# Optimization experiments

Measured on AMD Instinct MI355X. Metric: run time of the kernel, lower is better.

Reference implementation:

```python
import jax, jax.numpy as jnp
import numpy as np

N = 65536   # nodes
D = 64      # feature dim
K = 32      # top-k kept features per node (k_value)
DEG = 16    # average degree
E = N * DEG # edges


def setup_inputs() -> dict:
    key = jax.random.key(0)
    k1, k2, k3, k4, k5 = jax.random.split(key, 5)
    feat = jax.random.normal(k1, (N, D), dtype=jnp.float32)
    topk_values = jax.random.normal(k2, (N, K), dtype=jnp.float32)
    topk_indices = jax.random.randint(k3, (N, K), 0, D, dtype=jnp.int32)
    edge_src = jax.random.randint(k4, (E,), 0, N, dtype=jnp.int32)
    # sorted dst row ids == CSR row structure (expanded indptr)
    edge_dst = jnp.sort(jax.random.randint(k5, (E,), 0, N, dtype=jnp.int32))
    eps = jnp.zeros((1,), dtype=jnp.float32)  # init_eps=0, learn_eps=False
    return {"feat": feat, "topk_values": topk_values, "eps": eps,
            "topk_indices": topk_indices, "edge_src": edge_src, "edge_dst": edge_dst}


def reference(feat, topk_values, eps, topk_indices, edge_src, edge_dst):
    n, d = feat.shape
    # MaxK SpMM: reconstruct sparse (top-k compressed) dense features, then
    # CSR sum-aggregation with unit edge values (graph_values = ones).
    rows = jnp.arange(n, dtype=topk_indices.dtype)[:, None]        # [N,1]
    dense = jnp.zeros_like(feat).at[rows, topk_indices].add(topk_values)  # [N,D]
    # neigh[i] = sum_{j in N(i)} dense[j]
    neigh = jax.ops.segment_sum(dense[edge_src], edge_dst, num_segments=n)  # [N,D]
    # GIN update: (1 + eps) * feat_dst + neigh  (apply_func=None, activation=None)
    return (1.0 + eps) * feat + neigh
```

## Files before the change

kernel.cpp:

```cpp
#include <hip/hip_runtime.h>


#define DFEAT 64
#define KTOP  32

__device__ __forceinline__ unsigned short f2bf(float x) {
    unsigned u = __float_as_uint(x);
    u += 0x7fffu + ((u >> 16) & 1u);
    return (unsigned short)(u >> 16);
}
__device__ __forceinline__ float bfu(unsigned int u16) {
    return __uint_as_float(u16 << 16);
}

__global__ __launch_bounds__(256) void prep_kernel(
    const float* __restrict__ topk_v,
    const int*   __restrict__ topk_i,
    const int*   __restrict__ edge_dst,
    unsigned int* __restrict__ dense16,
    int*          __restrict__ indptr,
    int n_nodes, int n_edges)
{
    __shared__ float rows[4][2 * DFEAT];
    int tid    = blockIdx.x * blockDim.x + threadIdx.x;
    int stride = gridDim.x * blockDim.x;
    int lane   = threadIdx.x & 63;
    int wid    = threadIdx.x >> 6;
    int wave   = tid >> 6;
    int nwaves = stride >> 6;
    int half   = lane >> 5;

    for (int e = tid; e < n_edges; e += stride) {
        int cur  = edge_dst[e];
        int prev = (e == 0) ? -1 : edge_dst[e - 1];
        for (int node = prev + 1; node <= cur; ++node) indptr[node] = e;
        if (e == n_edges - 1) {
            for (int node = cur + 1; node <= n_nodes; ++node) indptr[node] = n_edges;
        }
    }

    int total_pairs = n_nodes >> 1;
    for (int pair = wave; pair < total_pairs; pair += nwaves) {
        int nodeA = pair * 2;

        rows[wid][lane]      = 0.0f;
        rows[wid][lane + 64] = 0.0f;

        size_t base = (size_t)nodeA * KTOP;
        int   idx = topk_i[base + lane];
        float val = topk_v[base + lane];
        atomicAdd(&rows[wid][half * DFEAT + idx], val);

        float a = rows[wid][2 * lane];
        float b = rows[wid][2 * lane + 1];
        dense16[nodeA * 32 + lane] =
            (unsigned int)f2bf(a) | ((unsigned int)f2bf(b) << 16);
    }
}

__global__ __launch_bounds__(256) void aggregate_bf16_kernel(
    const uint4*  __restrict__ d16q,
    const float4* __restrict__ feat4,
    const float*  __restrict__ eps,
    const int*    __restrict__ edge_src,
    const int*    __restrict__ indptr,
    float4*       __restrict__ out4,
    int n_nodes)
{
    int lane   = threadIdx.x & 63;
    int f      = lane & 7;
    int eg     = lane >> 3;
    int wave   = (blockIdx.x * blockDim.x + threadIdx.x) >> 6;
    int nwaves = (gridDim.x * blockDim.x) >> 6;
    float sc   = 1.0f + eps[0];

    for (int nA = wave; nA < n_nodes; nA += 2 * nwaves) {
        int nB = nA + nwaves;
        bool hasB = nB < n_nodes;

        int sA = indptr[nA],  eA = indptr[nA + 1];
        int sB = 0, eB = 0;
        if (hasB) { sB = indptr[nB]; eB = indptr[nB + 1]; }

        float4 ftA = make_float4(0, 0, 0, 0), ftB = make_float4(0, 0, 0, 0);
        if (eg < 2) {
            ftA = feat4[(size_t)nA * 16 + 2 * f + eg];
            if (hasB) ftB = feat4[(size_t)nB * 16 + 2 * f + eg];
        }

        float accA[8] = {0, 0, 0, 0, 0, 0, 0, 0};
        float accB[8] = {0, 0, 0, 0, 0, 0, 0, 0};

        int lenA = eA - sA, lenB = eB - sB;
        int lenM = lenA > lenB ? lenA : lenB;
        for (int off = 0; off < lenM; off += 16) {
#pragma unroll
            for (int u = 0; u < 2; ++u) {
                int ea = sA + off + 8 * u + eg;
                int eb = sB + off + 8 * u + eg;
                if (ea < eA) {
                    int s = edge_src[ea];
                    uint4 r = d16q[(size_t)s * 8 + f];
                    accA[0] += bfu(r.x & 0xffffu); accA[1] += bfu(r.x >> 16);
                    accA[2] += bfu(r.y & 0xffffu); accA[3] += bfu(r.y >> 16);
                    accA[4] += bfu(r.z & 0xffffu); accA[5] += bfu(r.z >> 16);
                    accA[6] += bfu(r.w & 0xffffu); accA[7] += bfu(r.w >> 16);
                }
                if (hasB && eb < eB) {
                    int s = edge_src[eb];
                    uint4 r = d16q[(size_t)s * 8 + f];
                    accB[0] += bfu(r.x & 0xffffu); accB[1] += bfu(r.x >> 16);
                    accB[2] += bfu(r.y & 0xffffu); accB[3] += bfu(r.y >> 16);
                    accB[4] += bfu(r.z & 0xffffu); accB[5] += bfu(r.z >> 16);
                    accB[6] += bfu(r.w & 0xffffu); accB[7] += bfu(r.w >> 16);
                }
            }
        }

#pragma unroll
        for (int d = 8; d < 64; d <<= 1) {
#pragma unroll
            for (int j = 0; j < 8; ++j) {
                accA[j] += __shfl_xor(accA[j], d, 64);
                accB[j] += __shfl_xor(accB[j], d, 64);
            }
        }

        if (eg < 2) {
            int q = eg * 4;
            float4 o;
            o.x = sc * ftA.x + accA[q + 0];
            o.y = sc * ftA.y + accA[q + 1];
            o.z = sc * ftA.z + accA[q + 2];
            o.w = sc * ftA.w + accA[q + 3];
            out4[(size_t)nA * 16 + 2 * f + eg] = o;
            if (hasB) {
                float4 p;
                p.x = sc * ftB.x + accB[q + 0];
                p.y = sc * ftB.y + accB[q + 1];
                p.z = sc * ftB.z + accB[q + 2];
                p.w = sc * ftB.w + accB[q + 3];
                out4[(size_t)nB * 16 + 2 * f + eg] = p;
            }
        }
    }
}

extern "C" void kernel_launch(void* const* d_in, const int* in_sizes, int n_in,
                              void* d_out, int out_size, void* d_ws, size_t ws_size,
                              hipStream_t stream)
{
    const float* feat     = (const float*)d_in[0];
    const float* topk_v   = (const float*)d_in[1];
    const float* eps      = (const float*)d_in[2];
    const int*   topk_i   = (const int*)d_in[3];
    const int*   edge_src = (const int*)d_in[4];
    const int*   edge_dst = (const int*)d_in[5];
    float*       out      = (float*)d_out;

    int n_nodes = in_sizes[0] / DFEAT;
    int n_edges = in_sizes[4];

    unsigned int* dense16 = (unsigned int*)d_ws;
    size_t d16_bytes = (size_t)n_nodes * DFEAT * sizeof(unsigned short);
    size_t d16_pad   = (d16_bytes + 255) & ~(size_t)255;
    int*   indptr    = (int*)((char*)d_ws + d16_pad);

    prep_kernel<<<2048, 256, 0, stream>>>(topk_v, topk_i, edge_dst,
                                          dense16, indptr, n_nodes, n_edges);
    aggregate_bf16_kernel<<<2048, 256, 0, stream>>>(
        (const uint4*)dense16, (const float4*)feat, eps, edge_src,
        indptr, (float4*)out, n_nodes);
}
```

Measured before the change: 126.1 us.

## Map eight-lane groups to single nodes in aggregation, dropping cross-lane reductions

The aggregation kernel changes from one wave handling two nodes, with edges spread across lane groups and combined by shuffle reductions, to each 8-lane group owning one node and looping over its edges serially. The grid is sized to the node count instead of grid-striding. This removes the shuffle-reduction overhead and the idle lanes during the output phase. In exchange, each lane group walks its edges one at a time with less memory-level parallelism per node, and different node degrees within a wave cause divergence.

```diff
diff --git a/kernel.cpp b/kernel.cpp
--- a/kernel.cpp
+++ b/kernel.cpp
@@ -67,83 +67,46 @@
     float4*       __restrict__ out4,
     int n_nodes)
 {
-    int lane   = threadIdx.x & 63;
-    int f      = lane & 7;
-    int eg     = lane >> 3;
-    int wave   = (blockIdx.x * blockDim.x + threadIdx.x) >> 6;
-    int nwaves = (gridDim.x * blockDim.x) >> 6;
-    float sc   = 1.0f + eps[0];
+    int lane = threadIdx.x & 63;
+    int f    = lane & 7;
+    int slot = lane >> 3;
+    int wave = (blockIdx.x * blockDim.x + threadIdx.x) >> 6;
+    int node = wave * 8 + slot;
+    if (node >= n_nodes) return;
 
-    for (int nA = wave; nA < n_nodes; nA += 2 * nwaves) {
-        int nB = nA + nwaves;
-        bool hasB = nB < n_nodes;
+    float sc = 1.0f + eps[0];
+    int s = indptr[node];
+    int e = indptr[node + 1];
 
-        int sA = indptr[nA],  eA = indptr[nA + 1];
-        int sB = 0, eB = 0;
-        if (hasB) { sB = indptr[nB]; eB = indptr[nB + 1]; }
-
-        float4 ftA = make_float4(0, 0, 0, 0), ftB = make_float4(0, 0, 0, 0);
-        if (eg < 2) {
-            ftA = feat4[(size_t)nA * 16 + 2 * f + eg];
-            if (hasB) ftB = feat4[(size_t)nB * 16 + 2 * f + eg];
-        }
-
-        float accA[8] = {0, 0, 0, 0, 0, 0, 0, 0};
-        float accB[8] = {0, 0, 0, 0, 0, 0, 0, 0};
-
-        int lenA = eA - sA, lenB = eB - sB;
-        int lenM = lenA > lenB ? lenA : lenB;
-        for (int off = 0; off < lenM; off += 16) {
+    float acc[8] = {0, 0, 0, 0, 0, 0, 0, 0};
+    for (int base = s; base < e; base += 4) {
 #pragma unroll
-            for (int u = 0; u < 2; ++u) {
-                int ea = sA + off + 8 * u + eg;
-                int eb = sB + off + 8 * u + eg;
-                if (ea < eA) {
-                    int s = edge_src[ea];
-                    uint4 r = d16q[(size_t)s * 8 + f];
-                    accA[0] += bfu(r.x & 0xffffu); accA[1] += bfu(r.x >> 16);
-                    accA[2] += bfu(r.y & 0xffffu); accA[3] += bfu(r.y >> 16);
-                    accA[4] += bfu(r.z & 0xffffu); accA[5] += bfu(r.z >> 16);
-                    accA[6] += bfu(r.w & 0xffffu); accA[7] += bfu(r.w >> 16);
-                }
-                if (hasB && eb < eB) {
-                    int s = edge_src[eb];
-                    uint4 r = d16q[(size_t)s * 8 + f];
-                    accB[0] += bfu(r.x & 0xffffu); accB[1] += bfu(r.x >> 16);
-                    accB[2] += bfu(r.y & 0xffffu); accB[3] += bfu(r.y >> 16);
-                    accB[4] += bfu(r.z & 0xffffu); accB[5] += bfu(r.z >> 16);
-                    accB[6] += bfu(r.w & 0xffffu); accB[7] += bfu(r.w >> 16);
-                }
-            }
-        }
-
-#pragma unroll
-        for (int d = 8; d < 64; d <<= 1) {
-#pragma unroll
-            for (int j = 0; j < 8; ++j) {
-                accA[j] += __shfl_xor(accA[j], d, 64);
-                accB[j] += __shfl_xor(accB[j], d, 64);
-            }
-        }
-
-        if (eg < 2) {
-            int q = eg * 4;
-            float4 o;
-            o.x = sc * ftA.x + accA[q + 0];
-            o.y = sc * ftA.y + accA[q + 1];
-            o.z = sc * ftA.z + accA[q + 2];
-            o.w = sc * ftA.w + accA[q + 3];
-            out4[(size_t)nA * 16 + 2 * f + eg] = o;
-            if (hasB) {
-                float4 p;
-                p.x = sc * ftB.x + accB[q + 0];
-                p.y = sc * ftB.y + accB[q + 1];
-                p.z = sc * ftB.z + accB[q + 2];
-                p.w = sc * ftB.w + accB[q + 3];
-                out4[(size_t)nB * 16 + 2 * f + eg] = p;
+        for (int u = 0; u < 4; ++u) {
+            int ee = base + u;
+            if (ee < e) {
+                int src = edge_src[ee];
+                uint4 r = d16q[(size_t)src * 8 + f];
+                acc[0] += bfu(r.x & 0xffffu); acc[1] += bfu(r.x >> 16);
+                acc[2] += bfu(r.y & 0xffffu); acc[3] += bfu(r.y >> 16);
+                acc[4] += bfu(r.z & 0xffffu); acc[5] += bfu(r.z >> 16);
+                acc[6] += bfu(r.w & 0xffffu); acc[7] += bfu(r.w >> 16);
             }
         }
     }
+
+    float4 ft0 = feat4[(size_t)node * 16 + 2 * f];
+    float4 ft1 = feat4[(size_t)node * 16 + 2 * f + 1];
+    float4 o0, o1;
+    o0.x = sc * ft0.x + acc[0];
+    o0.y = sc * ft0.y + acc[1];
+    o0.z = sc * ft0.z + acc[2];
+    o0.w = sc * ft0.w + acc[3];
+    o1.x = sc * ft1.x + acc[4];
+    o1.y = sc * ft1.y + acc[5];
+    o1.z = sc * ft1.z + acc[6];
+    o1.w = sc * ft1.w + acc[7];
+    out4[(size_t)node * 16 + 2 * f]     = o0;
+    out4[(size_t)node * 16 + 2 * f + 1] = o1;
 }
 
 extern "C" void kernel_launch(void* const* d_in, const int* in_sizes, int n_in,
@@ -168,7 +131,10 @@
 
     prep_kernel<<<2048, 256, 0, stream>>>(topk_v, topk_i, edge_dst,
                                           dense16, indptr, n_nodes, n_edges);
-    aggregate_bf16_kernel<<<2048, 256, 0, stream>>>(
+
+    int agg_waves  = (n_nodes + 7) / 8;
+    int agg_blocks = (agg_waves * 64 + 255) / 256;
+    aggregate_bf16_kernel<<<agg_blocks, 256, 0, stream>>>(
         (const uint4*)dense16, (const float4*)feat, eps, edge_src,
         indptr, (float4*)out, n_nodes);
 }
```

After: 124.5 us. About the same (-1.3%).
